# Performance work log

Measured on AMD Instinct MI355X. Metric: run time of the kernel, lower is better.

Reference implementation:

```python
import jax, jax.numpy as jnp
import numpy as np

B, L, N, D = 256, 32, 256 * 32, 768
NEG_INF = -1e30  # stand-in for float('-inf') that is safe under masking
SUPCON_W, REPULSION_W, BCE_W = 1.0, 0.1, 1.0
REPULSION_THRESHOLD = 0.3


def setup_inputs() -> dict:
    key = jax.random.key(0)
    k1, k2, k3 = jax.random.split(key, 3)
    logits = jax.random.normal(k1, (N, 1), dtype=jnp.float32)
    labels = jax.random.randint(k2, (B, L), 0, 2, dtype=jnp.int32)  # 0/1 targets
    batch_indices = jnp.arange(N, dtype=jnp.int64) // L   # each sample has L labels
    label_ids = jnp.arange(N, dtype=jnp.int64) % L + 1    # 1..L per sample
    label_embeddings = jax.random.normal(k3, (N, D), dtype=jnp.float32)
    logit_scale = jnp.full((1,), 2.0, dtype=jnp.float32)
    bce_scale = jnp.ones((1,), dtype=jnp.float32)
    return {
        "logits": logits, "labels": labels, "batch_indices": batch_indices,
        "label_ids": label_ids, "label_embeddings": label_embeddings,
        "logit_scale": logit_scale, "bce_scale": bce_scale,
    }


def _supcon_loss(dense_logits, targets):
    # targets: (B, L) float, -100 marks padding
    mask_valid = targets != -100.0
    targets_clean = jnp.where(mask_valid, targets, 0.0)
    pos_mask = (targets_clean > 0.5).astype(dense_logits.dtype)
    num_pos = pos_mask.sum(axis=1)                      # (B,)
    has_pos = num_pos > 0
    logits_masked = jnp.where(mask_valid, dense_logits, NEG_INF)
    log_probs = jax.nn.log_softmax(logits_masked, axis=1)
    sum_log_prob_pos = jnp.sum(jnp.where(pos_mask > 0, log_probs, 0.0), axis=1)
    loss_per_sample = -sum_log_prob_pos / (num_pos + 1e-9)
    n_anchor = jnp.maximum(has_pos.sum(), 1)
    return jnp.sum(jnp.where(has_pos, loss_per_sample, 0.0)) / n_anchor


def _label_repulsion_loss(embeddings, label_ids, batch_indices):
    norms = jnp.linalg.norm(embeddings, axis=-1, keepdims=True)
    emb_n = embeddings / jnp.maximum(norms, 1e-12)
    sim = emb_n @ emb_n.T                               # (N, N)
    mask = (label_ids[None, :] != label_ids[:, None]) & (
        batch_indices[None, :] == batch_indices[:, None])
    penalties = jax.nn.relu(sim - REPULSION_THRESHOLD)
    n_valid = jnp.maximum(mask.sum(), 1)
    return jnp.sum(jnp.where(mask, penalties, 0.0)) / n_valid


def _bce_loss(dense_logits, targets, logit_scale, bce_scale):
    mask = targets != -100.0
    raw = dense_logits / (jnp.exp(logit_scale[0]) + 1e-9)
    x = raw * jnp.maximum(jnp.abs(bce_scale[0]), 0.1)
    # stable BCE-with-logits: max(x,0) - x*t + log(1+exp(-|x|))
    per = jnp.maximum(x, 0.0) - x * targets + jnp.log1p(jnp.exp(-jnp.abs(x)))
    n_valid = jnp.maximum(mask.sum(), 1)
    return jnp.sum(jnp.where(mask, per, 0.0)) / n_valid


def reference(logits, labels, batch_indices, label_ids, label_embeddings,
              logit_scale, bce_scale):
    batch_size = labels.shape[0]
    max_label_id = L  # int(label_ids.max()); static here: label_ids span 1..L
    dense_logits = jnp.full((batch_size, max_label_id), NEG_INF, dtype=logits.dtype)
    dense_logits = dense_logits.at[batch_indices, label_ids - 1].set(logits[:, 0])
    targets = labels[:, :max_label_id].astype(jnp.float32)  # valid_cols == L
    total = jnp.float32(0.0)
    total = total + SUPCON_W * _supcon_loss(dense_logits, targets)
    total = total + REPULSION_W * _label_repulsion_loss(
        label_embeddings, label_ids, batch_indices)
    total = total + BCE_W * _bce_loss(dense_logits, targets, logit_scale, bce_scale)
    return total
```

## Files before the change

kernel.cpp:

```cpp
#include <hip/hip_runtime.h>
#include <hip/hip_bf16.h>
#include <math.h>

#define REP_N_VALID 253952.0f
#define BCE_N_VALID 8192.0f

#define KC 256
#define PITCH 260

__global__ __launch_bounds__(512) void fused_kernel(
        const float* __restrict__ emb,
        const float* __restrict__ logits, const int* __restrict__ labels,
        const float* __restrict__ logit_scale, const float* __restrict__ bce_scale,
        float4* __restrict__ partials) {
    __shared__ float tile[32 * PITCH];
    __shared__ float gram[32 * 32];
    __shared__ float inv_norm[32];
    __shared__ float wsum[8];
    __shared__ float rowres[3];

    const int t    = threadIdx.x;
    const int g    = blockIdx.x;
    const int w    = t >> 6;
    const int lane = t & 63;
    const int ty   = lane >> 3;
    const int tx   = lane & 7;

    float xval = 0.0f; float tgv = 0.0f;
    if (w == 0 && lane < 32) {
        xval = logits[g * 32 + lane];
        tgv  = (float)labels[g * 32 + lane];
    }

    for (int i = t; i < 1024; i += 512) gram[i] = 0.0f;

    float acc[4][4];
#pragma unroll
    for (int i = 0; i < 4; ++i)
#pragma unroll
        for (int j = 0; j < 4; ++j) acc[i][j] = 0.0f;

    const float* base = emb + (size_t)g * 32 * 768;

    for (int c = 0; c < 3; ++c) {
#pragma unroll
        for (int i = 0; i < 4; ++i) {
            int idx = t + i * 512;
            int row = idx >> 6;
            int c4  = idx & 63;
            float4 v = *(const float4*)(base + row * 768 + c * KC + c4 * 4);
            *(float4*)(&tile[row * PITCH + c4 * 4]) = v;
        }
        __syncthreads();

        const int k0 = w * 32;
#pragma unroll 1
        for (int s = 0; s < 8; ++s) {
            const int k = k0 + s * 4;
            float4 a[4], b[4];
#pragma unroll
            for (int r = 0; r < 4; ++r)
                a[r] = *(const float4*)(&tile[(ty + 8 * r) * PITCH + k]);
#pragma unroll
            for (int r = 0; r < 4; ++r)
                b[r] = *(const float4*)(&tile[(tx + 8 * r) * PITCH + k]);
#pragma unroll
            for (int i = 0; i < 4; ++i)
#pragma unroll
                for (int j = 0; j < 4; ++j) {
                    acc[i][j] = fmaf(a[i].x, b[j].x, acc[i][j]);
                    acc[i][j] = fmaf(a[i].y, b[j].y, acc[i][j]);
                    acc[i][j] = fmaf(a[i].z, b[j].z, acc[i][j]);
                    acc[i][j] = fmaf(a[i].w, b[j].w, acc[i][j]);
                }
        }
        __syncthreads();
    }

#pragma unroll
    for (int i = 0; i < 4; ++i)
#pragma unroll
        for (int j = 0; j < 4; ++j)
            atomicAdd(&gram[(ty + 8 * i) * 32 + (tx + 8 * j)], acc[i][j]);
    __syncthreads();

    if (t < 32) {
        float n = sqrtf(gram[t * 32 + t]);
        inv_norm[t] = 1.0f / fmaxf(n, 1e-12f);
    }

    if (w == 0 && lane < 32) {
        float m = xval;
#pragma unroll
        for (int off = 16; off > 0; off >>= 1) m = fmaxf(m, __shfl_xor(m, off, 32));
        float e = expf(xval - m);
        float se = e;
#pragma unroll
        for (int off = 16; off > 0; off >>= 1) se += __shfl_xor(se, off, 32);
        const float lse = logf(se) + m;

        const float inv_es = 1.0f / (expf(logit_scale[0]) + 1e-9f);
        const float bsc    = fmaxf(fabsf(bce_scale[0]), 0.1f);

        float pos  = (tgv > 0.5f) ? 1.0f : 0.0f;
        float slp  = pos * (xval - lse);
        float xx   = xval * inv_es * bsc;
        float bce  = fmaxf(xx, 0.0f) - xx * tgv + log1pf(expf(-fabsf(xx)));
        float npos = pos;
#pragma unroll
        for (int off = 16; off > 0; off >>= 1) {
            npos += __shfl_xor(npos, off, 32);
            slp  += __shfl_xor(slp,  off, 32);
            bce  += __shfl_xor(bce,  off, 32);
        }
        if (lane == 0) {
            rowres[0] = (npos > 0.0f) ? (-slp / (npos + 1e-9f)) : 0.0f;
            rowres[1] = (npos > 0.0f) ? 1.0f : 0.0f;
            rowres[2] = bce;
        }
    }
    __syncthreads();

    float psum = 0.0f;
#pragma unroll
    for (int rr = 0; rr < 2; ++rr) {
        int e = t + rr * 512;
        int i = e >> 5, j = e & 31;
        if (i != j) {
            float sim = gram[e] * inv_norm[i] * inv_norm[j];
            psum += fmaxf(sim - 0.3f, 0.0f);
        }
    }
#pragma unroll
    for (int off = 32; off > 0; off >>= 1) psum += __shfl_down(psum, off, 64);
    if (lane == 0) wsum[w] = psum;
    __syncthreads();

    if (t == 0) {
        float rep = wsum[0] + wsum[1] + wsum[2] + wsum[3]
                  + wsum[4] + wsum[5] + wsum[6] + wsum[7];
        partials[g] = make_float4(rep, rowres[0], rowres[1], rowres[2]);
    }
}

__global__ __launch_bounds__(256) void reduce_kernel(
        const float4* __restrict__ partials, float* __restrict__ out) {
    __shared__ float r0[4], r1[4], r2[4], r3[4];
    const int t = threadIdx.x;
    float4 p = partials[t];
    float v0 = p.x, v1 = p.y, v2 = p.z, v3 = p.w;
#pragma unroll
    for (int off = 32; off > 0; off >>= 1) {
        v0 += __shfl_down(v0, off, 64);
        v1 += __shfl_down(v1, off, 64);
        v2 += __shfl_down(v2, off, 64);
        v3 += __shfl_down(v3, off, 64);
    }
    const int wave = t >> 6;
    if ((t & 63) == 0) { r0[wave] = v0; r1[wave] = v1; r2[wave] = v2; r3[wave] = v3; }
    __syncthreads();
    if (t == 0) {
        float rep = r0[0] + r0[1] + r0[2] + r0[3];
        float sup = r1[0] + r1[1] + r1[2] + r1[3];
        float anc = r2[0] + r2[1] + r2[2] + r2[3];
        float bce = r3[0] + r3[1] + r3[2] + r3[3];
        out[0] = sup / fmaxf(anc, 1.0f)
               + 0.1f * (rep / REP_N_VALID)
               + bce / BCE_N_VALID;
    }
}

extern "C" void kernel_launch(void* const* d_in, const int* in_sizes, int n_in,
                              void* d_out, int out_size, void* d_ws, size_t ws_size,
                              hipStream_t stream) {
    const float* logits      = (const float*)d_in[0];
    const int*   labels      = (const int*)d_in[1];
    const float* emb         = (const float*)d_in[4];
    const float* logit_scale = (const float*)d_in[5];
    const float* bce_scale   = (const float*)d_in[6];
    float*  out      = (float*)d_out;
    float4* partials = (float4*)d_ws;

    fused_kernel<<<dim3(256), dim3(512), 0, stream>>>(emb, logits, labels,
                                                      logit_scale, bce_scale, partials);
    reduce_kernel<<<dim3(1), dim3(256), 0, stream>>>(partials, out);
}
```

Measured before the change: 102.4 us.

## Double-buffer embedding chunks with register prefetch and swizzled LDS Gram tiles

The per-group Gram computation is restructured. Global loads for the next K chunk are prefetched into registers while the current chunk is computed from a double-buffered LDS tile, using an XOR swizzle instead of padding to avoid bank conflicts. Each thread now computes an 8x8 output block over a K quarter, then reduces across lanes with shuffles and across waves through a per-wave shared partial buffer, replacing the LDS atomics. This cuts sync stalls and atomic traffic but raises register pressure (64 accumulators, launch bounds 512,2) and LDS use (about 100KB).

```diff
diff --git a/kernel.cpp b/kernel.cpp
--- a/kernel.cpp
+++ b/kernel.cpp
@@ -1,20 +1,63 @@
 #include <hip/hip_runtime.h>
-#include <hip/hip_bf16.h>
 #include <math.h>
 
 #define REP_N_VALID 253952.0f
 #define BCE_N_VALID 8192.0f
 
-#define KC 256
-#define PITCH 260
-
-__global__ __launch_bounds__(512) void fused_kernel(
+__device__ __forceinline__ int permf(int q) {
+    return (q & 4) | ((q & 1) << 1) | ((q >> 1) & 1);
+}
+
+__device__ __forceinline__ void stage_store(float* bufp, const float4 r[4],
+                                            int w, int lane) {
+#pragma unroll
+    for (int i = 0; i < 4; ++i) {
+        const int row = w + 8 * i;
+        *(float4*)&bufp[row * 256 + 4 * (lane ^ permf(row >> 2))] = r[i];
+    }
+}
+
+__device__ __forceinline__ void stage_load(float4 r[4], const float* base,
+                                           int c, int w, int lane) {
+#pragma unroll
+    for (int i = 0; i < 4; ++i)
+        r[i] = *(const float4*)(base + (size_t)(w + 8 * i) * 768 + c * 256 + lane * 4);
+}
+
+__device__ __forceinline__ void compute_chunk(const float* bufp, float (&acc)[8][8],
+                                              int w, int kq, int ty, int tx) {
+#pragma unroll
+    for (int s = 0; s < 2; ++s) {
+        const int c4 = w * 8 + kq * 2 + s;
+        float4 av[8], bv[8];
+#pragma unroll
+        for (int i = 0; i < 8; ++i)
+            av[i] = *(const float4*)&bufp[(8 * ty + i) * 256 +
+                                          4 * (c4 ^ permf(2 * ty + (i >> 2)))];
+#pragma unroll
+        for (int j = 0; j < 8; ++j)
+            bv[j] = *(const float4*)&bufp[(8 * tx + j) * 256 +
+                                          4 * (c4 ^ permf(2 * tx + (j >> 2)))];
+#pragma unroll
+        for (int i = 0; i < 8; ++i)
+#pragma unroll
+            for (int j = 0; j < 8; ++j) {
+                acc[i][j] = fmaf(av[i].x, bv[j].x, acc[i][j]);
+                acc[i][j] = fmaf(av[i].y, bv[j].y, acc[i][j]);
+                acc[i][j] = fmaf(av[i].z, bv[j].z, acc[i][j]);
+                acc[i][j] = fmaf(av[i].w, bv[j].w, acc[i][j]);
+            }
+    }
+}
+
+__global__ __launch_bounds__(512, 2) void fused_kernel(
         const float* __restrict__ emb,
         const float* __restrict__ logits, const int* __restrict__ labels,
         const float* __restrict__ logit_scale, const float* __restrict__ bce_scale,
         float4* __restrict__ partials) {
-    __shared__ float tile[32 * PITCH];
-    __shared__ float gram[32 * 32];
+    __shared__ float buf[2][32 * 256];
+    __shared__ float gram8[8 * 1024];
+    __shared__ float finalg[1024];
     __shared__ float inv_norm[32];
     __shared__ float wsum[8];
     __shared__ float rowres[3];
@@ -23,69 +66,74 @@
     const int g    = blockIdx.x;
     const int w    = t >> 6;
     const int lane = t & 63;
-    const int ty   = lane >> 3;
-    const int tx   = lane & 7;
-
-    float xval = 0.0f; float tgv = 0.0f;
+    const int kq   = lane >> 4;
+    const int ty   = (lane >> 2) & 3;
+    const int tx   = lane & 3;
+
+    float xval = 0.0f, tgv = 0.0f;
     if (w == 0 && lane < 32) {
         xval = logits[g * 32 + lane];
         tgv  = (float)labels[g * 32 + lane];
     }
 
-    for (int i = t; i < 1024; i += 512) gram[i] = 0.0f;
-
-    float acc[4][4];
-#pragma unroll
-    for (int i = 0; i < 4; ++i)
-#pragma unroll
-        for (int j = 0; j < 4; ++j) acc[i][j] = 0.0f;
+    float acc[8][8];
+#pragma unroll
+    for (int i = 0; i < 8; ++i)
+#pragma unroll
+        for (int j = 0; j < 8; ++j) acc[i][j] = 0.0f;
 
     const float* base = emb + (size_t)g * 32 * 768;
 
-    for (int c = 0; c < 3; ++c) {
-#pragma unroll
-        for (int i = 0; i < 4; ++i) {
-            int idx = t + i * 512;
-            int row = idx >> 6;
-            int c4  = idx & 63;
-            float4 v = *(const float4*)(base + row * 768 + c * KC + c4 * 4);
-            *(float4*)(&tile[row * PITCH + c4 * 4]) = v;
-        }
-        __syncthreads();
-
-        const int k0 = w * 32;
-#pragma unroll 1
-        for (int s = 0; s < 8; ++s) {
-            const int k = k0 + s * 4;
-            float4 a[4], b[4];
-#pragma unroll
-            for (int r = 0; r < 4; ++r)
-                a[r] = *(const float4*)(&tile[(ty + 8 * r) * PITCH + k]);
-#pragma unroll
-            for (int r = 0; r < 4; ++r)
-                b[r] = *(const float4*)(&tile[(tx + 8 * r) * PITCH + k]);
-#pragma unroll
-            for (int i = 0; i < 4; ++i)
-#pragma unroll
-                for (int j = 0; j < 4; ++j) {
-                    acc[i][j] = fmaf(a[i].x, b[j].x, acc[i][j]);
-                    acc[i][j] = fmaf(a[i].y, b[j].y, acc[i][j]);
-                    acc[i][j] = fmaf(a[i].z, b[j].z, acc[i][j]);
-                    acc[i][j] = fmaf(a[i].w, b[j].w, acc[i][j]);
-                }
-        }
-        __syncthreads();
-    }
-
-#pragma unroll
-    for (int i = 0; i < 4; ++i)
-#pragma unroll
-        for (int j = 0; j < 4; ++j)
-            atomicAdd(&gram[(ty + 8 * i) * 32 + (tx + 8 * j)], acc[i][j]);
+    float4 sA[4], sB[4];
+    stage_load(sA, base, 0, w, lane);
+    stage_load(sB, base, 1, w, lane);
+    stage_store(buf[0], sA, w, lane);
+    __syncthreads();
+
+    stage_load(sA, base, 2, w, lane);
+    stage_store(buf[1], sB, w, lane);
+    compute_chunk(buf[0], acc, w, kq, ty, tx);
+    __syncthreads();
+
+    stage_store(buf[0], sA, w, lane);
+    compute_chunk(buf[1], acc, w, kq, ty, tx);
+    __syncthreads();
+
+    compute_chunk(buf[0], acc, w, kq, ty, tx);
+
+#pragma unroll
+    for (int i = 0; i < 8; ++i)
+#pragma unroll
+        for (int j = 0; j < 8; ++j) {
+            float v = acc[i][j];
+            v += __shfl_xor(v, 16, 64);
+            v += __shfl_xor(v, 32, 64);
+            acc[i][j] = v;
+        }
+#pragma unroll
+    for (int i = 0; i < 8; ++i)
+        if (kq == (i >> 1)) {
+#pragma unroll
+            for (int jj = 0; jj < 2; ++jj)
+                *(float4*)&gram8[w * 1024 + (8 * ty + i) * 32 + 8 * tx + 4 * jj] =
+                    make_float4(acc[i][4 * jj + 0], acc[i][4 * jj + 1],
+                                acc[i][4 * jj + 2], acc[i][4 * jj + 3]);
+        }
+    __syncthreads();
+
+    if (t < 256) {
+        float4 s0 = *(const float4*)&gram8[t * 4];
+#pragma unroll
+        for (int ww = 1; ww < 8; ++ww) {
+            const float4 p = *(const float4*)&gram8[ww * 1024 + t * 4];
+            s0.x += p.x; s0.y += p.y; s0.z += p.z; s0.w += p.w;
+        }
+        *(float4*)&finalg[t * 4] = s0;
+    }
     __syncthreads();
 
     if (t < 32) {
-        float n = sqrtf(gram[t * 32 + t]);
+        float n = sqrtf(finalg[t * 32 + t]);
         inv_norm[t] = 1.0f / fmaxf(n, 1e-12f);
     }
 
@@ -127,7 +175,7 @@
         int e = t + rr * 512;
         int i = e >> 5, j = e & 31;
         if (i != j) {
-            float sim = gram[e] * inv_norm[i] * inv_norm[j];
+            float sim = finalg[e] * inv_norm[i] * inv_norm[j];
             psum += fmaxf(sim - 0.3f, 0.0f);
         }
     }
```

New measurement: 119.1 us. +16.3%, slower.
